# Optimization experiments

Hardware: AMD Instinct MI355X
Metric: run time of the kernel (lower is better)

Reference implementation:

```python
import jax, jax.numpy as jnp
import numpy as np

N_NODES = 50000
N_EDGES = 1600000
DIM_NODE = 64
DIM_HIDDEN = [64, 64]
EDGE_DIM = 32
NUM_CLASSES = 10
NUM_GRAPHS = 128


def _glorot(key, shape):
    fan_in, fan_out = shape[0], shape[1]
    lim = jnp.sqrt(6.0 / (fan_in + fan_out))
    return jax.random.uniform(key, shape, jnp.float32, -lim, lim)


def setup_inputs() -> dict:
    key = jax.random.key(0)
    ks = jax.random.split(key, 20)
    x = jax.random.normal(ks[0], (N_NODES, DIM_NODE), jnp.float32)
    edge_attr = jax.random.normal(ks[1], (N_EDGES, EDGE_DIM), jnp.float32)
    edge_index = jax.random.randint(ks[2], (2, N_EDGES), 0, N_NODES, jnp.int64)
    batch = jnp.sort(jax.random.randint(ks[3], (N_NODES,), 0, NUM_GRAPHS, jnp.int64))
    h0 = (DIM_NODE + DIM_HIDDEN[0]) // 2  # 64
    h1 = (DIM_HIDDEN[0] + DIM_HIDDEN[1]) // 2  # 64
    return {
        "x": x,
        "edge_attr": edge_attr,
        "We1": _glorot(ks[4], (EDGE_DIM, DIM_NODE)), "be1": jnp.zeros((DIM_NODE,), jnp.float32),
        "W1a": _glorot(ks[5], (DIM_NODE, h0)), "b1a": jnp.zeros((h0,), jnp.float32),
        "W1b": _glorot(ks[6], (h0, DIM_HIDDEN[0])), "b1b": jnp.zeros((DIM_HIDDEN[0],), jnp.float32),
        "We2": _glorot(ks[7], (EDGE_DIM, DIM_HIDDEN[0])), "be2": jnp.zeros((DIM_HIDDEN[0],), jnp.float32),
        "W2a": _glorot(ks[8], (DIM_HIDDEN[0], h1)), "b2a": jnp.zeros((h1,), jnp.float32),
        "W2b": _glorot(ks[9], (h1, DIM_HIDDEN[1])), "b2b": jnp.zeros((DIM_HIDDEN[1],), jnp.float32),
        "Wf": _glorot(ks[10], (DIM_HIDDEN[1], NUM_CLASSES)), "bf": jnp.zeros((NUM_CLASSES,), jnp.float32),
        "edge_index": edge_index,
        "batch": batch,
    }


def _gine_conv(x, edge_index, edge_attr, We, be, Wa, ba, Wb, bb):
    # PyG GINEConv (eps=0): msg = relu(x_src + lin_edge(edge_attr)),
    # aggr = scatter_sum(msg -> dst), out = nn(x + aggr)
    src, dst = edge_index[0], edge_index[1]
    e = edge_attr @ We + be                      # [E, d]
    m = jax.nn.relu(x[src] + e)                  # [E, d] gather + add + relu
    aggr = jax.ops.segment_sum(m, dst, num_segments=x.shape[0])  # [N, d]
    h = x + aggr
    h = h @ Wa + ba
    h = h @ Wb + bb
    return h


def reference(x, edge_attr, We1, be1, W1a, b1a, W1b, b1b,
              We2, be2, W2a, b2a, W2b, b2b, Wf, bf,
              edge_index, batch):
    h = jax.nn.relu(_gine_conv(x, edge_index, edge_attr, We1, be1, W1a, b1a, W1b, b1b))
    h = jax.nn.relu(_gine_conv(h, edge_index, edge_attr, We2, be2, W2a, b2a, W2b, b2b))
    # global mean pool per graph
    sums = jax.ops.segment_sum(h, batch, num_segments=NUM_GRAPHS)
    cnts = jax.ops.segment_sum(jnp.ones((h.shape[0],), h.dtype), batch, num_segments=NUM_GRAPHS)
    pooled = sums / jnp.clip(cnts, 1.0)[:, None]
    # ffn: (dropout p=0 in eval) -> linear -> softmax
    logits = pooled @ Wf + bf
    return jax.nn.softmax(logits, axis=1)
```

## Files before the change

### kernel.cpp

```cpp
#include <hip/hip_runtime.h>

#define N_NODES 50000
#define N_EDGES 1600000
#define DIM 64
#define EDIM 32
#define NUM_GRAPHS 128
#define NUM_CLASSES 10
#define NBIN_PAD 50176
#define NSCAN_BLK 196
#define EPAD_MAX 2200000
#define NBUCK 196
#define BCAP 12288
#define ACH 4096

typedef __attribute__((ext_vector_type(8))) short bf16x8;
typedef __attribute__((ext_vector_type(4))) short short4v;
typedef __attribute__((ext_vector_type(4))) float f32x4;

static __device__ __forceinline__ short f2bf(float f) {
    unsigned u = __builtin_bit_cast(unsigned, f);
    u += 0x7fff + ((u >> 16) & 1);
    return (short)(u >> 16);
}
static __device__ __forceinline__ float bf2f(short s) {
    unsigned u = ((unsigned)(unsigned short)s) << 16;
    return __builtin_bit_cast(float, u);
}
static __device__ __forceinline__ int cvt_pk_bf16(float lo, float hi) {
    int r;
    asm("v_cvt_pk_bf16_f32 %0, %1, %2" : "=v"(r) : "v"(lo), "v"(hi));
    return r;
}

__global__ void __launch_bounds__(256) binA_kernel(
    const int* __restrict__ src, const int* __restrict__ dst,
    int* __restrict__ bcur, int2* __restrict__ bbuf)
{
    __shared__ int hist[256];
    __shared__ int scanb[256];
    __shared__ int bexcl[256];
    __shared__ int cursA[256];
    __shared__ int gbase[256];
    __shared__ int2 st[ACH];

    const int t = threadIdx.x;
    const int e0 = blockIdx.x * ACH;
    const int nv = min(ACH, N_EDGES - e0);

    hist[t] = 0;
    __syncthreads();

    int w1[ACH / 256];
    #pragma unroll
    for (int i = 0; i < ACH / 256; ++i) {
        int idx = t + 256 * i;
        if (idx < nv) {
            int e = e0 + idx;
            int d = dst[e], s = src[e];
            w1[i] = (s & 0xFFFF) | (d << 16);
            atomicAdd(&hist[(unsigned)w1[i] >> 24], 1);
        } else {
            w1[i] = -1;
        }
    }
    __syncthreads();

    int v = hist[t];
    scanb[t] = v;
    __syncthreads();
    #pragma unroll
    for (int off = 1; off < 256; off <<= 1) {
        int add = (t >= off) ? scanb[t - off] : 0;
        __syncthreads();
        scanb[t] += add;
        __syncthreads();
    }
    int excl = scanb[t] - v;
    bexcl[t] = excl;
    cursA[t] = excl;
    if (v > 0) gbase[t] = atomicAdd(&bcur[t], v);
    __syncthreads();

    #pragma unroll
    for (int i = 0; i < ACH / 256; ++i) {
        int idx = t + 256 * i;
        if (idx < nv) {
            int b = (unsigned)w1[i] >> 24;
            int r = atomicAdd(&cursA[b], 1);
            int2 rec; rec.x = e0 + idx; rec.y = w1[i];
            st[r] = rec;
        }
    }
    __syncthreads();

    for (int k = t; k < nv; k += 256) {
        int2 rec = st[k];
        int b = (unsigned)rec.y >> 24;
        int pos = gbase[b] + (k - bexcl[b]);
        if (pos < BCAP) bbuf[(size_t)b * BCAP + pos] = rec;
    }
}

__global__ void __launch_bounds__(1024) binB1_kernel(
    const int* __restrict__ bcur, const int2* __restrict__ bbuf,
    int* __restrict__ cnt)
{
    __shared__ int nodecnt[256];
    const int b = blockIdx.x, t = threadIdx.x;
    if (t < 256) nodecnt[t] = 0;
    __syncthreads();
    const int nb = min(bcur[b], BCAP);
    for (int k = t; k < nb; k += 1024) {
        int2 rec = bbuf[(size_t)b * BCAP + k];
        int dlow = ((unsigned)rec.y >> 16) & 0xFF;
        atomicAdd(&nodecnt[dlow], 1);
    }
    __syncthreads();
    if (t < 256) cnt[b * 256 + t] = nodecnt[t];
}

__global__ void scan_part(const int* __restrict__ cnt, int* __restrict__ pstart,
                          int* __restrict__ partial) {
    __shared__ int sh[256];
    const int b = blockIdx.x, t = threadIdx.x;
    const int i = b * 256 + t;
    int v = ((cnt[i] + 15) >> 4) << 4;
    sh[t] = v;
    __syncthreads();
    #pragma unroll
    for (int off = 1; off < 256; off <<= 1) {
        int add = (t >= off) ? sh[t - off] : 0;
        __syncthreads();
        sh[t] += add;
        __syncthreads();
    }
    pstart[i] = sh[t] - v;
    if (t == 255) partial[b] = sh[t];
}

__global__ void scan_mid(int* __restrict__ partial) {
    __shared__ int sh[256];
    const int t = threadIdx.x;
    int v = (t < NSCAN_BLK) ? partial[t] : 0;
    sh[t] = v;
    __syncthreads();
    #pragma unroll
    for (int off = 1; off < 256; off <<= 1) {
        int add = (t >= off) ? sh[t - off] : 0;
        __syncthreads();
        sh[t] += add;
        __syncthreads();
    }
    if (t < NSCAN_BLK) partial[t] = sh[t] - v;
}

__global__ void scan_add(int* __restrict__ pstart, const int* __restrict__ partial) {
    const int b = blockIdx.x, t = threadIdx.x;
    const int i = b * 256 + t;
    pstart[i] += partial[b];
}

__global__ void __launch_bounds__(1024) binB2_kernel(
    const int* __restrict__ bcur, const int2* __restrict__ bbuf,
    const int* __restrict__ pstart, const int* __restrict__ cnt,
    int2* __restrict__ pes, int* __restrict__ tnode)
{
    __shared__ int cur[256];
    const int b = blockIdx.x, t = threadIdx.x;
    if (t < 256) cur[t] = pstart[b * 256 + t];
    __syncthreads();
    const int nb = min(bcur[b], BCAP);
    for (int k = t; k < nb; k += 1024) {
        int2 rec = bbuf[(size_t)b * BCAP + k];
        unsigned y = (unsigned)rec.y;
        int dlow = (y >> 16) & 0xFF;
        int p = atomicAdd(&cur[dlow], 1);
        int2 o; o.x = rec.x; o.y = (int)(y & 0xFFFF);
        pes[p] = o;
    }
    __syncthreads();
    if (t < 256) {
        int n = b * 256 + t;
        if (n < N_NODES) {
            int p0 = pstart[n], deg = cnt[n];
            int pe = p0 + (((deg + 15) >> 4) << 4);
            int2 pad; pad.x = -1; pad.y = N_NODES;
            for (int p = p0 + deg; p < pe; ++p) pes[p] = pad;
            for (int tt = p0 >> 4; tt < (pe >> 4); ++tt) tnode[tt] = n;
        }
    }
}

__global__ void xprep_kernel(const float* __restrict__ x, short* __restrict__ xb,
                             short* __restrict__ hb) {
    int t = blockIdx.x * blockDim.x + threadIdx.x;
    if (t >= (N_NODES + 1) * 64) return;
    int n = t >> 6, k = t & 63;
    if (n == N_NODES) {
        short pz = f2bf(-1e30f);
        xb[t] = pz;
        hb[t] = pz;
        return;
    }
    int dim = 16 * (k & 3) + (k >> 2);
    xb[(size_t)n * 64 + k] = f2bf(x[(size_t)n * 64 + dim]);
}

__global__ void __launch_bounds__(256) edge_kernel(
    const short* __restrict__ xb,
    const float* __restrict__ ea,
    const float* __restrict__ We,
    const float* __restrict__ be,
    const int2*  __restrict__ pes,
    const int*   __restrict__ tnode,
    const int*   __restrict__ pstart,
    float* __restrict__ aggr)
{
    const int lane = threadIdx.x & 63;
    const int q = lane >> 4;
    const int c = lane & 15;
    const int wave  = (blockIdx.x * blockDim.x + threadIdx.x) >> 6;
    const int nwav  = (gridDim.x * blockDim.x) >> 6;

    const int ntiles = pstart[N_NODES] >> 4;
    const int t0 = (int)(((long long)ntiles * wave) / nwav);
    const int t1 = (int)(((long long)ntiles * (wave + 1)) / nwav);
    if (t0 >= t1) return;

    bf16x8 bfrag[4];
    #pragma unroll
    for (int t = 0; t < 4; ++t) {
        #pragma unroll
        for (int e = 0; e < 8; ++e) {
            int k = 4 * q + (e & 3) + 16 * (e >> 2);
            bfrag[t][e] = f2bf(We[k * 64 + 16 * t + c]);
        }
    }
    f32x4 cb[4];
    #pragma unroll
    for (int t = 0; t < 4; ++t) {
        float bv = be[16 * t + c];
        cb[t][0] = bv; cb[t][1] = bv; cb[t][2] = bv; cb[t][3] = bv;
    }

    auto loadIdx = [&](int tt, int& tn, int& pm, int4& s4) {
        const int2* p = pes + (size_t)tt * 16;
        int4 a = *reinterpret_cast<const int4*>(p + 4 * q);
        int4 b = *reinterpret_cast<const int4*>(p + 4 * q + 2);
        tn = tnode[tt];
        pm = p[c].x;
        s4.x = a.y; s4.y = a.w; s4.z = b.y; s4.w = b.w;
    };
    auto loadEa = [&](int pm, float4& e0, float4& e1) {
        int ep = pm < 0 ? 0 : pm;
        const float* ar = ea + (size_t)ep * EDIM + 4 * q;
        e0 = *reinterpret_cast<const float4*>(ar);
        e1 = *reinterpret_cast<const float4*>(ar + 16);
    };
    auto loadXv = [&](const int4& s4, short4v& x0, short4v& x1,
                      short4v& x2, short4v& x3) {
        x0 = *reinterpret_cast<const short4v*>(xb + (size_t)s4.x * 64 + 4 * c);
        x1 = *reinterpret_cast<const short4v*>(xb + (size_t)s4.y * 64 + 4 * c);
        x2 = *reinterpret_cast<const short4v*>(xb + (size_t)s4.z * 64 + 4 * c);
        x3 = *reinterpret_cast<const short4v*>(xb + (size_t)s4.w * 64 + 4 * c);
    };

    int prev_n = -1;
    float acc0 = 0.f, acc1 = 0.f, acc2 = 0.f, acc3 = 0.f;

    auto flush = [&](int n) {
        float r0 = acc0 + __shfl_xor(acc0, 16, 64);
        float r1 = acc1 + __shfl_xor(acc1, 16, 64);
        float r2 = acc2 + __shfl_xor(acc2, 16, 64);
        float r3 = acc3 + __shfl_xor(acc3, 16, 64);
        r0 += __shfl_xor(r0, 32, 64);
        r1 += __shfl_xor(r1, 32, 64);
        r2 += __shfl_xor(r2, 32, 64);
        r3 += __shfl_xor(r3, 32, 64);
        float v = (q == 0) ? r0 : (q == 1) ? r1 : (q == 2) ? r2 : r3;
        float* dp = aggr + (size_t)n * 64 + lane;
        int a0 = pstart[n] >> 4, a1 = pstart[n + 1] >> 4;
        if (a0 >= t0 && a1 <= t1) *dp = v;
        else atomicAdd(dp, v);
    };

    int tn0, pm0, tn1, pm1, tn2, pm2;
    int4 s40, s41, s42;
    loadIdx(t0, tn0, pm0, s40);
    loadIdx(t0 + 1 < t1 ? t0 + 1 : t1 - 1, tn1, pm1, s41);
    loadIdx(t0 + 2 < t1 ? t0 + 2 : t1 - 1, tn2, pm2, s42);

    float4 ea00, ea01, ea10, ea11;
    short4v xv0, xv1, xv2, xv3;
    loadEa(pm0, ea00, ea01);
    loadEa(pm1, ea10, ea11);
    loadXv(s40, xv0, xv1, xv2, xv3);

    for (int tile = t0; tile < t1; ++tile) {
        float4 ea20, ea21;
        loadEa(pm2, ea20, ea21);
        short4v y0, y1, y2, y3;
        loadXv(s41, y0, y1, y2, y3);
        int tn3, pm3; int4 s43;
        loadIdx(tile + 3 < t1 ? tile + 3 : t1 - 1, tn3, pm3, s43);

        if (tn0 != prev_n) {
            if (prev_n >= 0) flush(prev_n);
            prev_n = tn0;
            acc0 = acc1 = acc2 = acc3 = 0.f;
        }

        int4 af;
        af.x = cvt_pk_bf16(ea00.x, ea00.y);
        af.y = cvt_pk_bf16(ea00.z, ea00.w);
        af.z = cvt_pk_bf16(ea01.x, ea01.y);
        af.w = cvt_pk_bf16(ea01.z, ea01.w);
        bf16x8 afrag = __builtin_bit_cast(bf16x8, af);

        f32x4 d[4];
        #pragma unroll
        for (int t = 0; t < 4; ++t)
            d[t] = __builtin_amdgcn_mfma_f32_16x16x32_bf16(afrag, bfrag[t], cb[t], 0, 0, 0);

        const short4v xv[4] = {xv0, xv1, xv2, xv3};
        #pragma unroll
        for (int r = 0; r < 4; ++r) {
            acc0 += fmaxf(d[0][r] + bf2f(xv[r][0]), 0.f);
            acc1 += fmaxf(d[1][r] + bf2f(xv[r][1]), 0.f);
            acc2 += fmaxf(d[2][r] + bf2f(xv[r][2]), 0.f);
            acc3 += fmaxf(d[3][r] + bf2f(xv[r][3]), 0.f);
        }

        tn0 = tn1; pm0 = pm1; s40 = s41;
        tn1 = tn2; pm1 = pm2; s41 = s42;
        tn2 = tn3; pm2 = pm3; s42 = s43;
        ea00 = ea10; ea01 = ea11;
        ea10 = ea20; ea11 = ea21;
        xv0 = y0; xv1 = y1; xv2 = y2; xv3 = y3;
    }
    if (prev_n >= 0) flush(prev_n);
}

__global__ void __launch_bounds__(256) node_kernel(
    const float* __restrict__ x,
    const float* __restrict__ aggr,
    const float* __restrict__ Wab,
    const float* __restrict__ bab,
    float* __restrict__ out,
    short* __restrict__ hb)
{
    const int lane = threadIdx.x & 63;
    const int q = lane >> 4;
    const int c = lane & 15;
    const int wave = (blockIdx.x * blockDim.x + threadIdx.x) >> 6;
    const int nwav = (gridDim.x * blockDim.x) >> 6;

    bf16x8 bfrag[2][4];
    #pragma unroll
    for (int kk = 0; kk < 2; ++kk) {
        #pragma unroll
        for (int t = 0; t < 4; ++t) {
            #pragma unroll
            for (int e = 0; e < 8; ++e) {
                int k = 32 * kk + 4 * q + (e & 3) + 16 * (e >> 2);
                bfrag[kk][t][e] = f2bf(Wab[k * 64 + 16 * t + c]);
            }
        }
    }
    f32x4 cb[4];
    #pragma unroll
    for (int t = 0; t < 4; ++t) {
        float bv = bab[16 * t + c];
        cb[t][0] = bv; cb[t][1] = bv; cb[t][2] = bv; cb[t][3] = bv;
    }

    const int ntile = N_NODES / 16;
    for (int nt = wave; nt < ntile; nt += nwav) {
        const int n0 = nt * 16;
        const float* xr = x    + (size_t)(n0 + c) * 64;
        const float* ar = aggr + (size_t)(n0 + c) * 64;
        float4 v[4];
        #pragma unroll
        for (int j = 0; j < 4; ++j) {
            int off = (j >> 1) * 32 + (j & 1) * 16 + 4 * q;
            float4 a = *reinterpret_cast<const float4*>(xr + off);
            float4 b = *reinterpret_cast<const float4*>(ar + off);
            v[j].x = a.x + b.x; v[j].y = a.y + b.y;
            v[j].z = a.z + b.z; v[j].w = a.w + b.w;
        }
        f32x4 d[4];
        #pragma unroll
        for (int kk = 0; kk < 2; ++kk) {
            int4 ai;
            ai.x = cvt_pk_bf16(v[2 * kk].x, v[2 * kk].y);
            ai.y = cvt_pk_bf16(v[2 * kk].z, v[2 * kk].w);
            ai.z = cvt_pk_bf16(v[2 * kk + 1].x, v[2 * kk + 1].y);
            ai.w = cvt_pk_bf16(v[2 * kk + 1].z, v[2 * kk + 1].w);
            bf16x8 afrag = __builtin_bit_cast(bf16x8, ai);
            #pragma unroll
            for (int t = 0; t < 4; ++t)
                d[t] = __builtin_amdgcn_mfma_f32_16x16x32_bf16(
                    afrag, bfrag[kk][t], kk == 0 ? cb[t] : d[t], 0, 0, 0);
        }
        #pragma unroll
        for (int r = 0; r < 4; ++r) {
            float h0 = fmaxf(d[0][r], 0.f);
            float h1v = fmaxf(d[1][r], 0.f);
            float h2v = fmaxf(d[2][r], 0.f);
            float h3 = fmaxf(d[3][r], 0.f);
            float* orow = out + (size_t)(n0 + 4 * q + r) * 64;
            orow[c]      = h0;
            orow[16 + c] = h1v;
            orow[32 + c] = h2v;
            orow[48 + c] = h3;
            int2 pk;
            pk.x = cvt_pk_bf16(h0, h1v);
            pk.y = cvt_pk_bf16(h2v, h3);
            *reinterpret_cast<int2*>(hb + (size_t)(n0 + 4 * q + r) * 64 + 4 * c) = pk;
        }
    }
}

__global__ void prep_kernel(
    const float* __restrict__ Wa1, const float* __restrict__ ba1,
    const float* __restrict__ Wb1, const float* __restrict__ bb1,
    const float* __restrict__ Wa2, const float* __restrict__ ba2,
    const float* __restrict__ Wb2, const float* __restrict__ bb2,
    float* __restrict__ Wab1, float* __restrict__ bab1,
    float* __restrict__ Wab2, float* __restrict__ bab2)
{
    const int t = threadIdx.x;
    for (int idx = t; idx < 64 * 64; idx += 256) {
        int i = idx >> 6, j = idx & 63;
        float s1 = 0.f, s2 = 0.f;
        for (int m = 0; m < 64; ++m) {
            s1 += Wa1[i * 64 + m] * Wb1[m * 64 + j];
            s2 += Wa2[i * 64 + m] * Wb2[m * 64 + j];
        }
        Wab1[idx] = s1; Wab2[idx] = s2;
    }
    for (int j = t; j < 64; j += 256) {
        float s1 = bb1[j], s2 = bb2[j];
        for (int m = 0; m < 64; ++m) {
            s1 += ba1[m] * Wb1[m * 64 + j];
            s2 += ba2[m] * Wb2[m * 64 + j];
        }
        bab1[j] = s1; bab2[j] = s2;
    }
}

__global__ void __launch_bounds__(256) pool_kernel(
    const float* __restrict__ h,
    const int*   __restrict__ batch,
    float* __restrict__ psum,
    float* __restrict__ pcnt)
{
    const int lane = threadIdx.x & 63;
    const int wave = (blockIdx.x * blockDim.x + threadIdx.x) >> 6;
    const int n0 = wave * 64;
    if (n0 >= N_NODES) return;
    const int nend = min(n0 + 64, N_NODES);

    int cur = batch[n0];
    float acc = 0.f;
    int cnt = 0;
    for (int n = n0; n < nend; ++n) {
        int b = batch[n];
        if (b != cur) {
            atomicAdd(&psum[(size_t)cur * 64 + lane], acc);
            if (lane == 0) atomicAdd(&pcnt[cur], (float)cnt);
            cur = b; acc = 0.f; cnt = 0;
        }
        acc += h[(size_t)n * 64 + lane];
        cnt++;
    }
    atomicAdd(&psum[(size_t)cur * 64 + lane], acc);
    if (lane == 0) atomicAdd(&pcnt[cur], (float)cnt);
}

__global__ void final_kernel(
    const float* __restrict__ psum, const float* __restrict__ pcnt,
    const float* __restrict__ Wf, const float* __restrict__ bfv,
    float* __restrict__ out)
{
    __shared__ float pooled[NUM_GRAPHS * 64];
    __shared__ float logits[NUM_GRAPHS * NUM_CLASSES];
    const int t = threadIdx.x;
    for (int idx = t; idx < NUM_GRAPHS * 64; idx += 256) {
        int g = idx >> 6;
        float cc = pcnt[g];
        cc = cc < 1.f ? 1.f : cc;
        pooled[idx] = psum[idx] / cc;
    }
    __syncthreads();
    for (int idx = t; idx < NUM_GRAPHS * NUM_CLASSES; idx += 256) {
        int g = idx / NUM_CLASSES, cc = idx % NUM_CLASSES;
        float acc = bfv[cc];
        for (int k = 0; k < 64; ++k)
            acc += pooled[g * 64 + k] * Wf[k * NUM_CLASSES + cc];
        logits[idx] = acc;
    }
    __syncthreads();
    if (t < NUM_GRAPHS) {
        float mx = -1e30f;
        for (int cc = 0; cc < NUM_CLASSES; ++cc)
            mx = fmaxf(mx, logits[t * NUM_CLASSES + cc]);
        float s = 0.f;
        float ex[NUM_CLASSES];
        for (int cc = 0; cc < NUM_CLASSES; ++cc) {
            ex[cc] = expf(logits[t * NUM_CLASSES + cc] - mx);
            s += ex[cc];
        }
        for (int cc = 0; cc < NUM_CLASSES; ++cc)
            out[t * NUM_CLASSES + cc] = ex[cc] / s;
    }
}

extern "C" void kernel_launch(void* const* d_in, const int* in_sizes, int n_in,
                              void* d_out, int out_size, void* d_ws, size_t ws_size,
                              hipStream_t stream) {
    const float* x   = (const float*)d_in[0];
    const float* ea  = (const float*)d_in[1];
    const float* We1 = (const float*)d_in[2];
    const float* be1 = (const float*)d_in[3];
    const float* W1a = (const float*)d_in[4];
    const float* b1a = (const float*)d_in[5];
    const float* W1b = (const float*)d_in[6];
    const float* b1b = (const float*)d_in[7];
    const float* We2 = (const float*)d_in[8];
    const float* be2 = (const float*)d_in[9];
    const float* W2a = (const float*)d_in[10];
    const float* b2a = (const float*)d_in[11];
    const float* W2b = (const float*)d_in[12];
    const float* b2b = (const float*)d_in[13];
    const float* Wf  = (const float*)d_in[14];
    const float* bfv = (const float*)d_in[15];
    const int* ei    = (const int*)d_in[16];
    const int* batch = (const int*)d_in[17];
    const int* src = ei;
    const int* dst = ei + N_EDGES;

    float* ws   = (float*)d_ws;
    float* aggr = ws;
    float* h1   = ws + 3200000;
    float* h2   = ws + 6400000;
    float* Wab1 = ws + 9600000;
    float* bab1 = Wab1 + 4096;
    float* Wab2 = bab1 + 64;
    float* bab2 = Wab2 + 4096;
    float* psum = bab2 + 64;
    float* pcnt = psum + 8192;
    int* cnt    = (int*)(pcnt + 128);
    int* pstart = cnt + NBIN_PAD;
    int* partial= pstart + NBIN_PAD;
    int* bcur   = partial + 256;
    int2* bbuf  = (int2*)(bcur + 256);
    int2* pes   = bbuf + (size_t)NBUCK * BCAP;
    int* tnode  = (int*)(pes + EPAD_MAX);
    short* xb   = (short*)(tnode + EPAD_MAX / 16);
    short* hb1  = xb + (size_t)(N_NODES + 1) * 64;
    short* hb2  = hb1 + (size_t)(N_NODES + 1) * 64;

    float* out = (float*)d_out;

    hipMemsetAsync(bcur, 0, 256 * sizeof(int), stream);
    binA_kernel<<<(N_EDGES + ACH - 1) / ACH, 256, 0, stream>>>(src, dst, bcur, bbuf);
    binB1_kernel<<<NBUCK, 1024, 0, stream>>>(bcur, bbuf, cnt);
    scan_part<<<NSCAN_BLK, 256, 0, stream>>>(cnt, pstart, partial);
    scan_mid<<<1, 256, 0, stream>>>(partial);
    scan_add<<<NSCAN_BLK, 256, 0, stream>>>(pstart, partial);
    binB2_kernel<<<NBUCK, 1024, 0, stream>>>(bcur, bbuf, pstart, cnt, pes, tnode);
    xprep_kernel<<<((N_NODES + 1) * 64 + 255) / 256, 256, 0, stream>>>(x, xb, hb1);

    hipMemsetAsync(psum, 0, (8192 + 128) * sizeof(float), stream);
    prep_kernel<<<1, 256, 0, stream>>>(W1a, b1a, W1b, b1b, W2a, b2a, W2b, b2b,
                                       Wab1, bab1, Wab2, bab2);

    hipMemsetAsync(aggr, 0, (size_t)N_NODES * DIM * sizeof(float), stream);
    edge_kernel<<<2048, 256, 0, stream>>>(xb, ea, We1, be1, pes, tnode, pstart, aggr);
    node_kernel<<<512, 256, 0, stream>>>(x, aggr, Wab1, bab1, h1, hb1);

    hipMemsetAsync(aggr, 0, (size_t)N_NODES * DIM * sizeof(float), stream);
    edge_kernel<<<2048, 256, 0, stream>>>(hb1, ea, We2, be2, pes, tnode, pstart, aggr);
    node_kernel<<<512, 256, 0, stream>>>(h1, aggr, Wab2, bab2, h2, hb2);

    pool_kernel<<<196, 256, 0, stream>>>(h2, batch, psum, pcnt);
    final_kernel<<<1, 256, 0, stream>>>(psum, pcnt, Wf, bfv, out);
}
```

Before: 344.9 us.

## Pre-permute edge attributes to bf16 in CSR order and drop atomics

During binning, edge attributes are converted to bf16 and written in destination-sorted, MFMA-fragment layout, so both edge passes stream contiguous bf16 data instead of gathering fp32 rows through an index. Source indices are stored as 16-bit values in place of int2 records. Wave tile ranges are extended to node boundaries so each node's aggregate is written by exactly one wave with plain stores, which removes the atomics and the two aggr memsets; nodes with zero degree are zeroed in binB2. The cost is a heavier binB2 with an extra bf16 edge buffer, and uint16 source indices only work because N_NODES is below 65536.

```diff
diff --git a/kernel.cpp b/kernel.cpp
--- a/kernel.cpp
+++ b/kernel.cpp
@@ -15,6 +15,7 @@
 
 typedef __attribute__((ext_vector_type(8))) short bf16x8;
 typedef __attribute__((ext_vector_type(4))) short short4v;
+typedef __attribute__((ext_vector_type(4))) unsigned short ushort4v;
 typedef __attribute__((ext_vector_type(4))) float f32x4;
 
 static __device__ __forceinline__ short f2bf(float f) {
@@ -163,7 +164,9 @@
 __global__ void __launch_bounds__(1024) binB2_kernel(
     const int* __restrict__ bcur, const int2* __restrict__ bbuf,
     const int* __restrict__ pstart, const int* __restrict__ cnt,
-    int2* __restrict__ pes, int* __restrict__ tnode)
+    const float* __restrict__ ea,
+    unsigned short* __restrict__ ssrc, short* __restrict__ eab,
+    int* __restrict__ tnode, float* __restrict__ aggr)
 {
     __shared__ int cur[256];
     const int b = blockIdx.x, t = threadIdx.x;
@@ -175,8 +178,20 @@
         unsigned y = (unsigned)rec.y;
         int dlow = (y >> 16) & 0xFF;
         int p = atomicAdd(&cur[dlow], 1);
-        int2 o; o.x = rec.x; o.y = (int)(y & 0xFFFF);
-        pes[p] = o;
+        ssrc[p] = (unsigned short)(y & 0xFFFF);
+        const float* ar = ea + (size_t)rec.x * EDIM;
+        int* er = (int*)(eab + (size_t)p * 32);
+        #pragma unroll
+        for (int qq = 0; qq < 4; ++qq) {
+            float4 lo = *reinterpret_cast<const float4*>(ar + 4 * qq);
+            float4 hi = *reinterpret_cast<const float4*>(ar + 4 * qq + 16);
+            int4 w;
+            w.x = cvt_pk_bf16(lo.x, lo.y);
+            w.y = cvt_pk_bf16(lo.z, lo.w);
+            w.z = cvt_pk_bf16(hi.x, hi.y);
+            w.w = cvt_pk_bf16(hi.z, hi.w);
+            *reinterpret_cast<int4*>(er + 4 * qq) = w;
+        }
     }
     __syncthreads();
     if (t < 256) {
@@ -184,9 +199,19 @@
         if (n < N_NODES) {
             int p0 = pstart[n], deg = cnt[n];
             int pe = p0 + (((deg + 15) >> 4) << 4);
-            int2 pad; pad.x = -1; pad.y = N_NODES;
-            for (int p = p0 + deg; p < pe; ++p) pes[p] = pad;
+            int4 z; z.x = 0; z.y = 0; z.z = 0; z.w = 0;
+            for (int p = p0 + deg; p < pe; ++p) {
+                ssrc[p] = (unsigned short)N_NODES;
+                int4* er = (int4*)(eab + (size_t)p * 32);
+                er[0] = z; er[1] = z; er[2] = z; er[3] = z;
+            }
             for (int tt = p0 >> 4; tt < (pe >> 4); ++tt) tnode[tt] = n;
+            if (deg == 0) {
+                float4 z4; z4.x = 0.f; z4.y = 0.f; z4.z = 0.f; z4.w = 0.f;
+                float4* arow = (float4*)(aggr + (size_t)n * 64);
+                #pragma unroll
+                for (int j = 0; j < 16; ++j) arow[j] = z4;
+            }
         }
     }
 }
@@ -208,10 +233,10 @@
 
 __global__ void __launch_bounds__(256) edge_kernel(
     const short* __restrict__ xb,
-    const float* __restrict__ ea,
+    const short* __restrict__ eab,
+    const unsigned short* __restrict__ ssrc,
     const float* __restrict__ We,
     const float* __restrict__ be,
-    const int2*  __restrict__ pes,
     const int*   __restrict__ tnode,
     const int*   __restrict__ pstart,
     float* __restrict__ aggr)
@@ -223,8 +248,10 @@
     const int nwav  = (gridDim.x * blockDim.x) >> 6;
 
     const int ntiles = pstart[N_NODES] >> 4;
-    const int t0 = (int)(((long long)ntiles * wave) / nwav);
-    const int t1 = (int)(((long long)ntiles * (wave + 1)) / nwav);
+    int t0 = (int)(((long long)ntiles * wave) / nwav);
+    int t1 = (int)(((long long)ntiles * (wave + 1)) / nwav);
+    while (t0 > 0 && t0 < ntiles && tnode[t0] == tnode[t0 - 1]) ++t0;
+    while (t1 > 0 && t1 < ntiles && tnode[t1] == tnode[t1 - 1]) ++t1;
     if (t0 >= t1) return;
 
     bf16x8 bfrag[4];
@@ -243,26 +270,13 @@
         cb[t][0] = bv; cb[t][1] = bv; cb[t][2] = bv; cb[t][3] = bv;
     }
 
-    auto loadIdx = [&](int tt, int& tn, int& pm, int4& s4) {
-        const int2* p = pes + (size_t)tt * 16;
-        int4 a = *reinterpret_cast<const int4*>(p + 4 * q);
-        int4 b = *reinterpret_cast<const int4*>(p + 4 * q + 2);
+    auto clampT = [&](int tt) { return tt < t1 ? tt : t1 - 1; };
+    auto loadIdx = [&](int tt, int& tn, ushort4v& s4) {
         tn = tnode[tt];
-        pm = p[c].x;
-        s4.x = a.y; s4.y = a.w; s4.z = b.y; s4.w = b.w;
+        s4 = *reinterpret_cast<const ushort4v*>(ssrc + tt * 16 + 4 * q);
     };
-    auto loadEa = [&](int pm, float4& e0, float4& e1) {
-        int ep = pm < 0 ? 0 : pm;
-        const float* ar = ea + (size_t)ep * EDIM + 4 * q;
-        e0 = *reinterpret_cast<const float4*>(ar);
-        e1 = *reinterpret_cast<const float4*>(ar + 16);
-    };
-    auto loadXv = [&](const int4& s4, short4v& x0, short4v& x1,
-                      short4v& x2, short4v& x3) {
-        x0 = *reinterpret_cast<const short4v*>(xb + (size_t)s4.x * 64 + 4 * c);
-        x1 = *reinterpret_cast<const short4v*>(xb + (size_t)s4.y * 64 + 4 * c);
-        x2 = *reinterpret_cast<const short4v*>(xb + (size_t)s4.z * 64 + 4 * c);
-        x3 = *reinterpret_cast<const short4v*>(xb + (size_t)s4.w * 64 + 4 * c);
+    auto loadE = [&](int tt) {
+        return *reinterpret_cast<const bf16x8*>(eab + (size_t)tt * 512 + c * 32 + q * 8);
     };
 
     int prev_n = -1;
@@ -278,51 +292,40 @@
         r2 += __shfl_xor(r2, 32, 64);
         r3 += __shfl_xor(r3, 32, 64);
         float v = (q == 0) ? r0 : (q == 1) ? r1 : (q == 2) ? r2 : r3;
-        float* dp = aggr + (size_t)n * 64 + lane;
-        int a0 = pstart[n] >> 4, a1 = pstart[n + 1] >> 4;
-        if (a0 >= t0 && a1 <= t1) *dp = v;
-        else atomicAdd(dp, v);
+        aggr[(size_t)n * 64 + lane] = v;
     };
 
-    int tn0, pm0, tn1, pm1, tn2, pm2;
-    int4 s40, s41, s42;
-    loadIdx(t0, tn0, pm0, s40);
-    loadIdx(t0 + 1 < t1 ? t0 + 1 : t1 - 1, tn1, pm1, s41);
-    loadIdx(t0 + 2 < t1 ? t0 + 2 : t1 - 1, tn2, pm2, s42);
-
-    float4 ea00, ea01, ea10, ea11;
-    short4v xv0, xv1, xv2, xv3;
-    loadEa(pm0, ea00, ea01);
-    loadEa(pm1, ea10, ea11);
-    loadXv(s40, xv0, xv1, xv2, xv3);
+    int tnA, tnB;
+    ushort4v s4A, s4B;
+    loadIdx(t0, tnA, s4A);
+    loadIdx(clampT(t0 + 1), tnB, s4B);
+    bf16x8 efA = loadE(t0);
+    short4v xvA0 = *reinterpret_cast<const short4v*>(xb + (size_t)s4A.x * 64 + 4 * c);
+    short4v xvA1 = *reinterpret_cast<const short4v*>(xb + (size_t)s4A.y * 64 + 4 * c);
+    short4v xvA2 = *reinterpret_cast<const short4v*>(xb + (size_t)s4A.z * 64 + 4 * c);
+    short4v xvA3 = *reinterpret_cast<const short4v*>(xb + (size_t)s4A.w * 64 + 4 * c);
 
     for (int tile = t0; tile < t1; ++tile) {
-        float4 ea20, ea21;
-        loadEa(pm2, ea20, ea21);
-        short4v y0, y1, y2, y3;
-        loadXv(s41, y0, y1, y2, y3);
-        int tn3, pm3; int4 s43;
-        loadIdx(tile + 3 < t1 ? tile + 3 : t1 - 1, tn3, pm3, s43);
-
-        if (tn0 != prev_n) {
+        bf16x8 efB = loadE(clampT(tile + 1));
+        short4v yv0 = *reinterpret_cast<const short4v*>(xb + (size_t)s4B.x * 64 + 4 * c);
+        short4v yv1 = *reinterpret_cast<const short4v*>(xb + (size_t)s4B.y * 64 + 4 * c);
+        short4v yv2 = *reinterpret_cast<const short4v*>(xb + (size_t)s4B.z * 64 + 4 * c);
+        short4v yv3 = *reinterpret_cast<const short4v*>(xb + (size_t)s4B.w * 64 + 4 * c);
+        int tnC; ushort4v s4C;
+        loadIdx(clampT(tile + 2), tnC, s4C);
+
+        if (tnA != prev_n) {
             if (prev_n >= 0) flush(prev_n);
-            prev_n = tn0;
+            prev_n = tnA;
             acc0 = acc1 = acc2 = acc3 = 0.f;
         }
 
-        int4 af;
-        af.x = cvt_pk_bf16(ea00.x, ea00.y);
-        af.y = cvt_pk_bf16(ea00.z, ea00.w);
-        af.z = cvt_pk_bf16(ea01.x, ea01.y);
-        af.w = cvt_pk_bf16(ea01.z, ea01.w);
-        bf16x8 afrag = __builtin_bit_cast(bf16x8, af);
-
         f32x4 d[4];
         #pragma unroll
         for (int t = 0; t < 4; ++t)
-            d[t] = __builtin_amdgcn_mfma_f32_16x16x32_bf16(afrag, bfrag[t], cb[t], 0, 0, 0);
-
-        const short4v xv[4] = {xv0, xv1, xv2, xv3};
+            d[t] = __builtin_amdgcn_mfma_f32_16x16x32_bf16(efA, bfrag[t], cb[t], 0, 0, 0);
+
+        const short4v xv[4] = {xvA0, xvA1, xvA2, xvA3};
         #pragma unroll
         for (int r = 0; r < 4; ++r) {
             acc0 += fmaxf(d[0][r] + bf2f(xv[r][0]), 0.f);
@@ -331,12 +334,10 @@
             acc3 += fmaxf(d[3][r] + bf2f(xv[r][3]), 0.f);
         }
 
-        tn0 = tn1; pm0 = pm1; s40 = s41;
-        tn1 = tn2; pm1 = pm2; s41 = s42;
-        tn2 = tn3; pm2 = pm3; s42 = s43;
-        ea00 = ea10; ea01 = ea11;
-        ea10 = ea20; ea11 = ea21;
-        xv0 = y0; xv1 = y1; xv2 = y2; xv3 = y3;
+        tnA = tnB; s4A = s4B;
+        tnB = tnC; s4B = s4C;
+        efA = efB;
+        xvA0 = yv0; xvA1 = yv1; xvA2 = yv2; xvA3 = yv3;
     }
     if (prev_n >= 0) flush(prev_n);
 }
@@ -540,11 +541,18 @@
     const int* src = ei;
     const int* dst = ei + N_EDGES;
 
-    float* ws   = (float*)d_ws;
-    float* aggr = ws;
-    float* h1   = ws + 3200000;
-    float* h2   = ws + 6400000;
-    float* Wab1 = ws + 9600000;
+    int* wsb = (int*)d_ws;
+    float* aggr = (float*)wsb;
+    float* h1   = (float*)(wsb + 3200000);
+    float* h2   = (float*)(wsb + 6400000);
+    short* eab  = (short*)(wsb + 9600000);
+    int2*  bbuf = (int2*)(wsb + 44800000);
+    short* xb   = (short*)(wsb + 49616896);
+    short* hb1  = (short*)(wsb + 51216928);
+    short* hb2  = (short*)(wsb + 52816960);
+    unsigned short* ssrc = (unsigned short*)(wsb + 54416992);
+    int* tnode  = wsb + 55516992;
+    float* Wab1 = (float*)(wsb + 55654492);
     float* bab1 = Wab1 + 4096;
     float* Wab2 = bab1 + 64;
     float* bab2 = Wab2 + 4096;
@@ -554,12 +562,6 @@
     int* pstart = cnt + NBIN_PAD;
     int* partial= pstart + NBIN_PAD;
     int* bcur   = partial + 256;
-    int2* bbuf  = (int2*)(bcur + 256);
-    int2* pes   = bbuf + (size_t)NBUCK * BCAP;
-    int* tnode  = (int*)(pes + EPAD_MAX);
-    short* xb   = (short*)(tnode + EPAD_MAX / 16);
-    short* hb1  = xb + (size_t)(N_NODES + 1) * 64;
-    short* hb2  = hb1 + (size_t)(N_NODES + 1) * 64;
 
     float* out = (float*)d_out;
 
@@ -569,19 +571,18 @@
     scan_part<<<NSCAN_BLK, 256, 0, stream>>>(cnt, pstart, partial);
     scan_mid<<<1, 256, 0, stream>>>(partial);
     scan_add<<<NSCAN_BLK, 256, 0, stream>>>(pstart, partial);
-    binB2_kernel<<<NBUCK, 1024, 0, stream>>>(bcur, bbuf, pstart, cnt, pes, tnode);
+    binB2_kernel<<<NBUCK, 1024, 0, stream>>>(bcur, bbuf, pstart, cnt, ea,
+                                             ssrc, eab, tnode, aggr);
     xprep_kernel<<<((N_NODES + 1) * 64 + 255) / 256, 256, 0, stream>>>(x, xb, hb1);
 
     hipMemsetAsync(psum, 0, (8192 + 128) * sizeof(float), stream);
     prep_kernel<<<1, 256, 0, stream>>>(W1a, b1a, W1b, b1b, W2a, b2a, W2b, b2b,
                                        Wab1, bab1, Wab2, bab2);
 
-    hipMemsetAsync(aggr, 0, (size_t)N_NODES * DIM * sizeof(float), stream);
-    edge_kernel<<<2048, 256, 0, stream>>>(xb, ea, We1, be1, pes, tnode, pstart, aggr);
+    edge_kernel<<<2048, 256, 0, stream>>>(xb, eab, ssrc, We1, be1, tnode, pstart, aggr);
     node_kernel<<<512, 256, 0, stream>>>(x, aggr, Wab1, bab1, h1, hb1);
 
-    hipMemsetAsync(aggr, 0, (size_t)N_NODES * DIM * sizeof(float), stream);
-    edge_kernel<<<2048, 256, 0, stream>>>(hb1, ea, We2, be2, pes, tnode, pstart, aggr);
+    edge_kernel<<<2048, 256, 0, stream>>>(hb1, eab, ssrc, We2, be2, tnode, pstart, aggr);
     node_kernel<<<512, 256, 0, stream>>>(h1, aggr, Wab2, bab2, h2, hb2);
 
     pool_kernel<<<196, 256, 0, stream>>>(h2, batch, psum, pcnt);
```

Measured after the change: 396.6 us. 1.15x slower.
